# Kernel tuning notes

Hardware: AMD Instinct MI355X
Metric: run time of the kernel (lower is better)

Reference implementation:

```python
import jax, jax.numpy as jnp
import numpy as np

B, S, H, V = 32, 128, 1024, 32000


def setup_inputs() -> dict:
    key = jax.random.key(0)
    ks = jax.random.split(key, 20)
    sc = 1.0 / np.sqrt(H)
    inp = {
        "inputs": jax.random.randint(ks[0], (B, S), 0, V),
        "annotations": jax.random.normal(ks[1], (B, S, H), dtype=jnp.float32),
        "hidden_init": jax.random.normal(ks[2], (B, H), dtype=jnp.float32),
        "E": jax.random.normal(ks[3], (V, H), dtype=jnp.float32) * sc,
        "Wxr": jax.random.normal(ks[4], (H, H), dtype=jnp.float32) * sc,
        "bxr": jnp.zeros((H,), jnp.float32),
        "Wxz": jax.random.normal(ks[5], (H, H), dtype=jnp.float32) * sc,
        "bxz": jnp.zeros((H,), jnp.float32),
        "Wxg": jax.random.normal(ks[6], (H, H), dtype=jnp.float32) * sc,
        "bxg": jnp.zeros((H,), jnp.float32),
        "Whr": jax.random.normal(ks[7], (H, H), dtype=jnp.float32) * sc,
        "bhr": jnp.zeros((H,), jnp.float32),
        "Whz": jax.random.normal(ks[8], (H, H), dtype=jnp.float32) * sc,
        "bhz": jnp.zeros((H,), jnp.float32),
        "Whg": jax.random.normal(ks[9], (H, H), dtype=jnp.float32) * sc,
        "bhg": jnp.zeros((H,), jnp.float32),
        "Wout": jax.random.normal(ks[10], (H, V), dtype=jnp.float32) * sc,
        "bout": jnp.zeros((V,), jnp.float32),
    }
    return inp


def reference(inputs, annotations, hidden_init, E, Wxr, bxr, Wxz, bxz, Wxg, bxg,
              Whr, bhr, Whz, bhz, Whg, bhg, Wout, bout):
    # annotations is unused (matches original non-attentional decoder).
    emb = E[inputs]  # [B, S, H]
    # Precompute all input-to-hidden projections as batched GEMMs (time-parallel).
    xr = jnp.einsum('bsh,hk->bsk', emb, Wxr) + bxr  # [B,S,H]
    xz = jnp.einsum('bsh,hk->bsk', emb, Wxz) + bxz
    xg = jnp.einsum('bsh,hk->bsk', emb, Wxg) + bxg
    # Scan over time for the sequential recurrence.
    xs = (jnp.swapaxes(xr, 0, 1), jnp.swapaxes(xz, 0, 1), jnp.swapaxes(xg, 0, 1))  # [S,B,H]

    def step(h, x):
        x_r, x_z, x_g = x
        r = jax.nn.sigmoid(x_r + h @ Whr + bhr)
        z = jax.nn.sigmoid(x_z + h @ Whz + bhz)
        g = jnp.tanh(x_g + r * (h @ Whg + bhg))
        h_new = (1.0 - z) * g + z * h
        return h_new, h_new

    _, hiddens = jax.lax.scan(step, hidden_init, xs)  # [S,B,H]
    hiddens = jnp.swapaxes(hiddens, 0, 1)  # [B,S,H]
    output = jnp.einsum('bsh,hv->bsv', hiddens, Wout) + bout  # [B,S,V]
    return output
```

## Files before the change

### kernel.cpp

```cpp
#include <hip/hip_runtime.h>
#include <hip/hip_bf16.h>

#define B_ 32
#define S_ 128
#define H_ 1024
#define V_ 32000

using short8 = __attribute__((ext_vector_type(8))) short;
using f32x4  = __attribute__((ext_vector_type(4))) float;
using u32x4  = __attribute__((ext_vector_type(4))) unsigned;
typedef unsigned short u16;

__device__ inline u16 f2bf(float f) {
  unsigned u = __float_as_uint(f);
  unsigned r = u + 0x7FFFu + ((u >> 16) & 1u);
  return (u16)(r >> 16);
}
__device__ inline float bf2f(u16 h) { return __uint_as_float(((unsigned)h) << 16); }

__device__ inline void gload_lds16(const void* g, void* l) {
  __builtin_amdgcn_global_load_lds((const __attribute__((address_space(1))) unsigned int*)g,
                                   (__attribute__((address_space(3))) unsigned int*)l, 16, 0, 0);
}
__device__ inline void gload_lds16_sc(const void* g, void* l) {
  __builtin_amdgcn_global_load_lds((const __attribute__((address_space(1))) unsigned int*)g,
                                   (__attribute__((address_space(3))) unsigned int*)l, 16, 0, 17);
}


__global__ void k_prep_all(const int* __restrict__ idx, const float* __restrict__ E,
                           u16* __restrict__ embf,
                           const float* __restrict__ Wxr, const float* __restrict__ Wxz,
                           const float* __restrict__ Wxg, u16* __restrict__ wxf,
                           const float* __restrict__ Whr, const float* __restrict__ Whz,
                           const float* __restrict__ Whg, u16* __restrict__ whh,
                           u16* __restrict__ whl,
                           const float* __restrict__ h0, unsigned* __restrict__ hpack,
                           int* __restrict__ sync,
                           const float* __restrict__ bxr, const float* __restrict__ bxz,
                           const float* __restrict__ bxg, float* __restrict__ bcat) {
  int gg = blockIdx.x * blockDim.x + threadIdx.x;
  if (gg < 524288) {
    int g = gg;
    int kt = g >> 14, rem = g & 16383, mt = rem >> 6, l = rem & 63;
    int row = mt * 16 + (l & 15);
    int k = kt * 32 + ((l >> 4) << 3);
    const float4* src = reinterpret_cast<const float4*>(E + (size_t)idx[row] * H_ + k);
    float4 a = src[0], b = src[1];
    u16 o[8] = {f2bf(a.x), f2bf(a.y), f2bf(a.z), f2bf(a.w),
                f2bf(b.x), f2bf(b.y), f2bf(b.z), f2bf(b.w)};
    *reinterpret_cast<uint4*>(embf + (size_t)g * 8) = *reinterpret_cast<const uint4*>(o);
  } else if (gg < 917504) {
    int g = gg - 524288;
    int kt = g / 12288, rem = g % 12288, nf = rem >> 6, l = rem & 63;
    int col = nf * 16 + (l & 15);
    int gate = col >> 10, j = col & 1023;
    int k0 = kt * 32 + ((l >> 4) << 3);
    const float* W = gate == 0 ? Wxr : (gate == 1 ? Wxz : Wxg);
    u16 o[8];
#pragma unroll
    for (int e = 0; e < 8; ++e) o[e] = f2bf(W[(size_t)(k0 + e) * H_ + j]);
    *reinterpret_cast<uint4*>(wxf + (size_t)g * 8) = *reinterpret_cast<const uint4*>(o);
  } else if (gg < 1310720) {
    int g = gg - 917504;
    int jtile = g / 6144, rem = g % 6144;
    int gate = rem >> 11, kt = (rem >> 6) & 31, l = rem & 63;
    int col = jtile * 16 + (l & 15);
    int k0 = kt * 32 + ((l >> 4) << 3);
    const float* W = gate == 0 ? Whr : (gate == 1 ? Whz : Whg);
    u16 oh[8], ol[8];
#pragma unroll
    for (int e = 0; e < 8; ++e) {
      float v = W[(size_t)(k0 + e) * H_ + col];
      u16 hi = f2bf(v);
      oh[e] = hi;
      ol[e] = f2bf(v - bf2f(hi));
    }
    *reinterpret_cast<uint4*>(whh + (size_t)g * 8) = *reinterpret_cast<const uint4*>(oh);
    *reinterpret_cast<uint4*>(whl + (size_t)g * 8) = *reinterpret_cast<const uint4*>(ol);
  } else if (gg < 1343488) {
    int i = gg - 1310720;
    float v = h0[i];
    u16 hi = f2bf(v);
    hpack[i] = (unsigned)hi | ((unsigned)f2bf(v - bf2f(hi)) << 16);
    if (i < 8192) sync[i] = 0;
  } else if (gg < 1346560) {
    int j = gg - 1343488;
    bcat[j] = j < 1024 ? bxr[j] : (j < 2048 ? bxz[j - 1024] : bxg[j - 2048]);
  }
}

template <int NTSTORE>
__launch_bounds__(256, 3)
__global__ void k_gemm_frag(const u16* __restrict__ Af, const u16* __restrict__ Bf,
                            const float* __restrict__ bias, float* __restrict__ C,
                            int MT, int NT, int KT, int N) {
  __shared__ __align__(16) u16 lA[2 * 512 * 8];
  __shared__ __align__(16) u16 lB[2 * 512 * 8];
  int tid = threadIdx.x, w = tid >> 6, lane = tid & 63;
  int mt0 = blockIdx.x * 8, nf0 = blockIdx.y * 8;
  int wm = (w >> 1) * 4, wn = (w & 1) * 4;
  f32x4 acc[4][4] = {};
  for (int kt = 0; kt < KT; kt += 2) {
    __syncthreads();
#pragma unroll
    for (int hh = 0; hh < 2; ++hh) {
      const u16* ga = Af + ((size_t)(kt + hh) * MT + mt0) * 512;
      const u16* gb = Bf + ((size_t)(kt + hh) * NT + nf0) * 512;
#pragma unroll
      for (int r = 0; r < 2; ++r) {
        int ub = (r * 4 + w) * 64;
        gload_lds16(ga + (size_t)(ub + lane) * 8, lA + (size_t)(hh * 512 + ub) * 8);
        gload_lds16(gb + (size_t)(ub + lane) * 8, lB + (size_t)(hh * 512 + ub) * 8);
      }
    }
    __syncthreads();
#pragma unroll
    for (int hh = 0; hh < 2; ++hh) {
      short8 af[4], bfr[4];
#pragma unroll
      for (int i = 0; i < 4; ++i) {
        af[i]  = *reinterpret_cast<const short8*>(lA + ((hh * 8 + wm + i) * 64 + lane) * 8);
        bfr[i] = *reinterpret_cast<const short8*>(lB + ((hh * 8 + wn + i) * 64 + lane) * 8);
      }
#pragma unroll
      for (int mi = 0; mi < 4; ++mi)
#pragma unroll
        for (int ni = 0; ni < 4; ++ni)
          acc[mi][ni] = __builtin_amdgcn_mfma_f32_16x16x32_bf16(af[mi], bfr[ni], acc[mi][ni], 0, 0, 0);
    }
  }
  int m0 = mt0 * 16, n0 = nf0 * 16;
#pragma unroll
  for (int ni = 0; ni < 4; ++ni) {
    int col = n0 + (wn + ni) * 16 + (lane & 15);
    float bv = bias[col];
#pragma unroll
    for (int mi = 0; mi < 4; ++mi) {
#pragma unroll
      for (int q = 0; q < 4; ++q) {
        int row = m0 + (wm + mi) * 16 + ((lane >> 4) << 2) + q;
        float v = acc[mi][ni][q] + bv;
        if (NTSTORE) __builtin_nontemporal_store(v, &C[(size_t)row * N + col]);
        else         C[(size_t)row * N + col] = v;
      }
    }
  }
}

__launch_bounds__(768, 3)
__global__ void k_gru_persist(const u16* __restrict__ whh, const u16* __restrict__ whl,
                              const float* __restrict__ xcat, const float* __restrict__ bhr,
                              const float* __restrict__ bhz, const float* __restrict__ bhg,
                              const float* __restrict__ hinit, unsigned* __restrict__ hpack,
                              u16* __restrict__ hiddf, int* __restrict__ sync,
                              const float* __restrict__ Wout, u16* __restrict__ wof) {
  __shared__ unsigned hstage[16][1028];
  __shared__ float red[3][4][16][16];
  const int bid = (int)blockIdx.x;
  const int tid = threadIdx.x;

  if (bid >= 128) {
    for (int g = (bid - 128) * 768 + tid; g < 4096000; g += 128 * 768) {
      int kt = g / 128000, rem = g - kt * 128000, nf = rem >> 6, l2 = rem & 63;
      int col = nf * 16 + (l2 & 15);
      int k0 = kt * 32 + ((l2 >> 4) << 3);
      u16 o[8];
#pragma unroll
      for (int e = 0; e < 8; ++e)
        o[e] = f2bf(__builtin_nontemporal_load(&Wout[(size_t)(k0 + e) * V_ + col]));
      *reinterpret_cast<uint4*>(wof + (size_t)g * 8) = *reinterpret_cast<const uint4*>(o);
    }
    return;
  }

  const int w = tid >> 6, l = tid & 63;
  const int mhalf = bid >> 6, jtile = bid & 63;
  const int gate = w >> 2, kg = w & 3;
  const int lr = l & 15, lc = (l >> 4) << 3;

  short8 bh[8], bl[8];
  {
    size_t wb = (size_t)(jtile * 3 + gate) * 32 * 512;
#pragma unroll
    for (int t = 0; t < 8; ++t) {
      size_t u = wb + ((size_t)(kg * 8 + t) * 64 + l) * 8;
      bh[t] = *reinterpret_cast<const short8*>(whh + u);
      bl[t] = *reinterpret_cast<const short8*>(whl + u);
    }
  }
#pragma unroll
  for (int t = 0; t < 8; ++t)
    asm volatile("" : "+v"(bh[t]), "+v"(bl[t]));

  const int erow = tid >> 4, ecol = tid & 15;
  const int eb = mhalf * 16 + erow, ej = jtile * 16 + ecol;
  const float* xp = xcat + (size_t)eb * S_ * 3072 + ej;
  float hprev = 0.f, br = 0.f, bz = 0.f, bg = 0.f, xr = 0.f, xz = 0.f, xg = 0.f;
  if (tid < 256) {
    hprev = hinit[(size_t)eb * H_ + ej];
    br = bhr[ej]; bz = bhz[ej]; bg = bhg[ej];
    xr = xp[0]; xz = xp[1024]; xg = xp[2048];
  }

  for (int s = 0; s < S_; ++s) {
    const int pi = s & 1, po = pi ^ 1;

    {
      const unsigned* hbase = hpack + (size_t)pi * (B_ * H_) + (size_t)(mhalf * 16) * H_;
      for (int c = w; c < 64; c += 12) {
        int r = c >> 2, q = c & 3;
        gload_lds16_sc(hbase + (size_t)r * H_ + q * 256 + l * 4, &hstage[r][q * 256]);
      }
    }
    __syncthreads();

    float nxr = 0.f, nxz = 0.f, nxg = 0.f;
    if (tid < 256 && s + 1 < S_) {
      const float* xq = xp + (size_t)(s + 1) * 3072;
      nxr = xq[0]; nxz = xq[1024]; nxg = xq[2048];
    }

    f32x4 acc = {};
#pragma unroll
    for (int t = 0; t < 8; ++t) {
      int c = (kg * 8 + t) * 32 + lc;
      uint4 A  = *reinterpret_cast<const uint4*>(&hstage[lr][c]);
      uint4 Bv = *reinterpret_cast<const uint4*>(&hstage[lr][c + 4]);
      union { unsigned u[4]; short8 s8; } ah, al;
      ah.u[0] = __builtin_amdgcn_perm(A.y, A.x, 0x05040100);
      al.u[0] = __builtin_amdgcn_perm(A.y, A.x, 0x07060302);
      ah.u[1] = __builtin_amdgcn_perm(A.w, A.z, 0x05040100);
      al.u[1] = __builtin_amdgcn_perm(A.w, A.z, 0x07060302);
      ah.u[2] = __builtin_amdgcn_perm(Bv.y, Bv.x, 0x05040100);
      al.u[2] = __builtin_amdgcn_perm(Bv.y, Bv.x, 0x07060302);
      ah.u[3] = __builtin_amdgcn_perm(Bv.w, Bv.z, 0x05040100);
      al.u[3] = __builtin_amdgcn_perm(Bv.w, Bv.z, 0x07060302);
      acc = __builtin_amdgcn_mfma_f32_16x16x32_bf16(ah.s8, bh[t], acc, 0, 0, 0);
      acc = __builtin_amdgcn_mfma_f32_16x16x32_bf16(ah.s8, bl[t], acc, 0, 0, 0);
      acc = __builtin_amdgcn_mfma_f32_16x16x32_bf16(al.s8, bh[t], acc, 0, 0, 0);
    }
#pragma unroll
    for (int q = 0; q < 4; ++q)
      red[gate][kg][(l >> 4) * 4 + q][lr] = acc[q];
    __syncthreads();

    if (tid < 256) {
      float ar = br + xr, az = bz + xz, ag = bg;
#pragma unroll
      for (int k2 = 0; k2 < 4; ++k2) {
        ar += red[0][k2][erow][ecol];
        az += red[1][k2][erow][ecol];
        ag += red[2][k2][erow][ecol];
      }
      float r = 1.f / (1.f + __expf(-ar));
      float z = 1.f / (1.f + __expf(-az));
      float ta = xg + r * ag;
      float gv = 1.f - 2.f / (__expf(2.f * ta) + 1.f);
      float hnew = (1.f - z) * gv + z * hprev;
      hprev = hnew;
      u16 hi = f2bf(hnew);
      u16 lo = f2bf(hnew - bf2f(hi));
      __hip_atomic_store(hpack + (size_t)po * (B_ * H_) + (size_t)eb * H_ + ej,
                         (unsigned)hi | ((unsigned)lo << 16),
                         __ATOMIC_RELAXED, __HIP_MEMORY_SCOPE_AGENT);
      int row = eb * S_ + s;
      int ktO = ej >> 5, mtO = row >> 4, laneO = (row & 15) + 16 * ((ej >> 3) & 3);
      hiddf[(((size_t)ktO * 256 + mtO) * 64 + laneO) * 8 + (ej & 7)] = hi;
    }
    xr = nxr; xz = nxz; xg = nxg;

    if (s + 1 < S_) {
      __syncthreads();
      if (tid == 0)
        __hip_atomic_store(sync + bid * 16, s + 1,
                           __ATOMIC_RELAXED, __HIP_MEMORY_SCOPE_AGENT);
      if (tid < 64) {
        const int* fp = sync + (mhalf * 64 + tid) * 16;
        while (__hip_atomic_load(fp, __ATOMIC_RELAXED, __HIP_MEMORY_SCOPE_AGENT) <= s)
          __builtin_amdgcn_s_sleep(1);
      }
      __syncthreads();
    }
  }
}

extern "C" void kernel_launch(void* const* d_in, const int* in_sizes, int n_in,
                              void* d_out, int out_size, void* d_ws, size_t ws_size,
                              hipStream_t stream) {
  const int*   inputs      = (const int*)d_in[0];
  const float* hidden_init = (const float*)d_in[2];
  const float* E    = (const float*)d_in[3];
  const float* Wxr  = (const float*)d_in[4];  const float* bxr = (const float*)d_in[5];
  const float* Wxz  = (const float*)d_in[6];  const float* bxz = (const float*)d_in[7];
  const float* Wxg  = (const float*)d_in[8];  const float* bxg = (const float*)d_in[9];
  const float* Whr  = (const float*)d_in[10]; const float* bhr = (const float*)d_in[11];
  const float* Whz  = (const float*)d_in[12]; const float* bhz = (const float*)d_in[13];
  const float* Whg  = (const float*)d_in[14]; const float* bhg = (const float*)d_in[15];
  const float* Wout = (const float*)d_in[16]; const float* bout = (const float*)d_in[17];
  float* out = (float*)d_out;

  char* ws = (char*)d_ws;
  u16* wxf       = (u16*)(ws);
  u16* wof       = (u16*)(ws + 6291456);
  u16* embf      = (u16*)(ws + 71827456);
  u16* hiddf     = embf;
  float* bcat    = (float*)(ws + 80216064);
  float* xcat    = (float*)(ws + 80228352);
  u16* whh       = (u16*)(ws + 130560000);
  u16* whl       = (u16*)(ws + 136851456);
  unsigned* hpack= (unsigned*)(ws + 143142912);
  int* syncb     = (int*)(ws + 143405056);

  k_prep_all<<<5261, 256, 0, stream>>>(inputs, E, embf, Wxr, Wxz, Wxg, wxf,
                                       Whr, Whz, Whg, whh, whl,
                                       hidden_init, hpack, syncb,
                                       bxr, bxz, bxg, bcat);

  k_gemm_frag<0><<<dim3(32, 24), 256, 0, stream>>>(embf, wxf, bcat, xcat, 256, 192, 32, 3072);

  {
    const u16* whh_p = whh; const u16* whl_p = whl; const float* xcat_p = xcat;
    const float* bhr_p = bhr; const float* bhz_p = bhz; const float* bhg_p = bhg;
    const float* hinit_p = hidden_init; unsigned* hpack_p = hpack;
    u16* hiddf_p = hiddf; int* sync_p = syncb;
    const float* wout_p = Wout; u16* wof_p = wof;
    void* kargs[] = {&whh_p, &whl_p, &xcat_p, &bhr_p, &bhz_p, &bhg_p,
                     &hinit_p, &hpack_p, &hiddf_p, &sync_p, &wout_p, &wof_p};
    hipLaunchCooperativeKernel((const void*)k_gru_persist, dim3(256), dim3(768),
                               kargs, 0, stream);
  }

  k_gemm_frag<1><<<dim3(32, 250), 256, 0, stream>>>(hiddf, wof, bout, out, 256, 2000, 32, 32000);
}
```

Measured before the change: 744.0 us.

## Replace output projection GEMM with 256x256-tile double-buffered 8-wave kernel

Adds a new bf16 MFMA GEMM kernel for the final hidden-to-vocab projection. It uses 256x256 block tiles with 512 threads and double-buffered direct-to-LDS global loads. Each K step is split into four phases that interleave the next tile's loads with MFMA work, using barriers and s_setprio. The larger tile is meant to cut global and LDS traffic per flop and to hide load latency. In exchange it uses more LDS and registers per block, leaves fewer blocks in the grid, and relies on fragile manual vmcnt accounting.

```diff
diff --git a/kernel.cpp b/kernel.cpp
--- a/kernel.cpp
+++ b/kernel.cpp
@@ -148,6 +148,88 @@
   }
 }
 
+__launch_bounds__(512, 2)
+__global__ void k_gemm256p(const u16* __restrict__ Af, const u16* __restrict__ Bf,
+                           const float* __restrict__ bias, float* __restrict__ C,
+                           int MT, int NTt, int KT2, int N) {
+  __shared__ __align__(16) u16 lA[2][2][16 * 512];
+  __shared__ __align__(16) u16 lB[2][2][16 * 512];
+  const int tid = threadIdx.x, w = tid >> 6, l = tid & 63;
+  const int mt0 = blockIdx.x * 16, nf0 = blockIdx.y * 16;
+  const int wm = (w & 1) * 8, wn = (w >> 1) * 4;
+  f32x4 acc[8][4] = {};
+
+#define STG_A(buf_, t_, kth_) {                                                    \
+    const u16* g0 = Af + ((size_t)(2 * (t_) + (kth_)) * MT + mt0) * 512;           \
+    gload_lds16(g0 + (size_t)tid * 8,         &lA[buf_][kth_][(size_t)tid * 8]);   \
+    gload_lds16(g0 + (size_t)(512 + tid) * 8, &lA[buf_][kth_][(size_t)(512 + tid) * 8]); }
+#define STG_B(buf_, t_, kth_) {                                                    \
+    const u16* g0 = Bf + ((size_t)(2 * (t_) + (kth_)) * NTt + nf0) * 512;          \
+    gload_lds16(g0 + (size_t)tid * 8,         &lB[buf_][kth_][(size_t)tid * 8]);   \
+    gload_lds16(g0 + (size_t)(512 + tid) * 8, &lB[buf_][kth_][(size_t)(512 + tid) * 8]); }
+
+  STG_A(0, 0, 0); STG_B(0, 0, 0);
+  STG_A(0, 0, 1); STG_B(0, 0, 1);
+  asm volatile("s_waitcnt vmcnt(4)" ::: "memory");
+  __builtin_amdgcn_s_barrier();
+
+#define PHASE(kth_, mth_, STG_STMT, WAIT_STMT)                                     \
+  {                                                                                \
+    short8 afr[4];                                                                 \
+    _Pragma("unroll") for (int i = 0; i < 4; ++i)                                  \
+      afr[i] = *reinterpret_cast<const short8*>(                                   \
+          &lA[cur][kth_][((size_t)(wm + (mth_) * 4 + i) * 64 + l) * 8]);           \
+    if ((mth_) == 0) {                                                             \
+      _Pragma("unroll") for (int i = 0; i < 4; ++i)                                \
+        bfr[i] = *reinterpret_cast<const short8*>(                                 \
+            &lB[cur][kth_][((size_t)(wn + i) * 64 + l) * 8]);                      \
+    }                                                                              \
+    STG_STMT;                                                                      \
+    WAIT_STMT;                                                                     \
+    __builtin_amdgcn_s_barrier();                                                  \
+    asm volatile("s_waitcnt lgkmcnt(0)" ::: "memory");                             \
+    __builtin_amdgcn_sched_barrier(0);                                             \
+    __builtin_amdgcn_s_setprio(1);                                                 \
+    _Pragma("unroll") for (int i = 0; i < 4; ++i)                                  \
+      _Pragma("unroll") for (int j = 0; j < 4; ++j)                                \
+        acc[(mth_) * 4 + i][j] = __builtin_amdgcn_mfma_f32_16x16x32_bf16(          \
+            afr[i], bfr[j], acc[(mth_) * 4 + i][j], 0, 0, 0);                      \
+    __builtin_amdgcn_s_setprio(0);                                                 \
+    __builtin_amdgcn_s_barrier();                                                  \
+  }
+
+  for (int t = 0; t < KT2; ++t) {
+    const int cur = t & 1, nxt = cur ^ 1;
+    const bool last = (t == KT2 - 1);
+    short8 bfr[4];
+    PHASE(0, 0, if (!last) STG_A(nxt, t + 1, 0), );
+    PHASE(0, 1, if (!last) STG_B(nxt, t + 1, 0),
+          if (!last) { asm volatile("s_waitcnt vmcnt(4)" ::: "memory"); }
+          else       { asm volatile("s_waitcnt vmcnt(0)" ::: "memory"); });
+    PHASE(1, 0, if (!last) STG_A(nxt, t + 1, 1), );
+    PHASE(1, 1, if (!last) STG_B(nxt, t + 1, 1),
+          if (!last) { asm volatile("s_waitcnt vmcnt(4)" ::: "memory"); });
+  }
+#undef PHASE
+#undef STG_A
+#undef STG_B
+
+  const int m0 = mt0 * 16, n0 = nf0 * 16;
+#pragma unroll
+  for (int ni = 0; ni < 4; ++ni) {
+    int col = n0 + (wn + ni) * 16 + (l & 15);
+    float bv = bias[col];
+#pragma unroll
+    for (int mi = 0; mi < 8; ++mi) {
+#pragma unroll
+      for (int q = 0; q < 4; ++q) {
+        int row = m0 + (wm + mi) * 16 + ((l >> 4) << 2) + q;
+        __builtin_nontemporal_store(acc[mi][ni][q] + bv, &C[(size_t)row * N + col]);
+      }
+    }
+  }
+}
+
 __launch_bounds__(768, 3)
 __global__ void k_gru_persist(const u16* __restrict__ whh, const u16* __restrict__ whl,
                               const float* __restrict__ xcat, const float* __restrict__ bhr,
@@ -331,5 +413,5 @@
                                kargs, 0, stream);
   }
 
-  k_gemm_frag<1><<<dim3(32, 250), 256, 0, stream>>>(hiddf, wof, bout, out, 256, 2000, 32, 32000);
-}
+  k_gemm256p<<<dim3(16, 125), 512, 0, stream>>>(hiddf, wof, bout, out, 256, 2000, 16, 32000);
+}
```

New measurement: 810.3 us. 8.9% more time.
